# Performance work log

Measured on AMD Instinct MI355X. Metric: run time of the kernel, lower is better.

## Reference

```python
import jax, jax.numpy as jnp
import numpy as np

N = 16384
RANK = 10
IN_F = 64
OUT_F = 64


def setup_inputs() -> dict:
    key = jax.random.key(0)
    k1, k2, k3, k4, k5 = jax.random.split(key, 5)
    return {
        "x": jax.random.normal(k1, (N, IN_F), dtype=jnp.float32),
        "source_embed": jax.random.normal(k2, (N, RANK), dtype=jnp.float32),
        "target_embed": jax.random.normal(k3, (RANK, N), dtype=jnp.float32),
        "W": jax.random.normal(k4, (OUT_F, IN_F), dtype=jnp.float32) * 0.1,
        "b": jax.random.normal(k5, (OUT_F,), dtype=jnp.float32) * 0.1,
    }


def reference(x, source_embed, target_embed, W, b):
    # Learned adjacency: [N, N] = softmax(relu(source @ target), row-wise)
    scores = jax.nn.relu(source_embed @ target_embed)  # [N, N]
    adj = jax.nn.softmax(scores, axis=1)               # [N, N]
    # Graph conv then linear (torch Linear: x @ W.T + b)
    agg = adj @ x                                       # [N, IN_F]
    return agg @ W.T + b                                # [N, OUT_F]
```

## Files before the change

### kernel.cpp

```cpp
#include <hip/hip_runtime.h>


constexpr int N    = 16384;
constexpr int RANK = 10;
constexpr int F    = 64;
constexpr int NH   = N / 2;

typedef float f32x4 __attribute__((ext_vector_type(4)));
typedef short bf16x8 __attribute__((ext_vector_type(8)));

constexpr float LOG2E = 1.4426950408889634f;

static __device__ __forceinline__ float fexp2(float x) {
    float r;
    asm("v_exp_f32 %0, %1" : "=v"(r) : "v"(x));
    return r;
}
static __device__ __forceinline__ unsigned short bfbits(float f) {
    return __builtin_bit_cast(unsigned short, (__bf16)f);
}

__global__ __launch_bounds__(256)
void prep(const float* __restrict__ x, const float* __restrict__ W,
          const float* __restrict__ te,
          uint4* __restrict__ yfrag, uint4* __restrict__ tefrag,
          int js0, int jt0)
{
    const int tid  = threadIdx.x;
    const int lane = tid & 63;
    const int g = lane >> 4, il = lane & 15;

    if (blockIdx.x < 256) {
        __shared__ float xs[32][68];
        const int jl = blockIdx.x;
        const int js = js0 + jl;
#pragma unroll
        for (int i = 0; i < 2; ++i) {
            const int fi = tid * 2 + i;
            const int r = fi >> 4, c4 = fi & 15;
            const float4 v = *reinterpret_cast<const float4*>(x + (size_t)(js * 32 + r) * F + c4 * 4);
            *reinterpret_cast<float4*>(&xs[r][c4 * 4]) = v;
        }
        __syncthreads();
        const int t = tid >> 6;
        const int f = t * 16 + il;
        float y[8];
#pragma unroll
        for (int b = 0; b < 8; ++b) y[b] = 0.f;
        const float* wr = W + f * F;
#pragma unroll
        for (int k4 = 0; k4 < F / 4; ++k4) {
            const float4 wv = *reinterpret_cast<const float4*>(wr + 4 * k4);
#pragma unroll
            for (int b = 0; b < 8; ++b) {
                const int row = 16 * (b >> 2) + 4 * g + (b & 3);
                const float4 xv = *reinterpret_cast<const float4*>(&xs[row][4 * k4]);
                y[b] = fmaf(xv.x, wv.x, y[b]);
                y[b] = fmaf(xv.y, wv.y, y[b]);
                y[b] = fmaf(xv.z, wv.z, y[b]);
                y[b] = fmaf(xv.w, wv.w, y[b]);
            }
        }
        union { unsigned short us[8]; uint4 v; } pk;
#pragma unroll
        for (int b = 0; b < 8; ++b) pk.us[b] = bfbits(y[b]);
        yfrag[(jl * 4 + t) * 64 + lane] = pk.v;
    } else {
        const int lt = (blockIdx.x - 256) * 4 + (tid >> 6);
        const int jt = jt0 + lt;
        union { unsigned short us[8]; uint4 v; } pk;
#pragma unroll
        for (int b = 0; b < 8; ++b) {
            const int k = 8 * g + b;
            unsigned short o = 0;
            if (k < 30) {
                const int band = (k < 10) ? 0 : (k < 20 ? 1 : 2);
                const int r = k - band * 10;
                const float v = te[r * N + jt * 16 + il];
                const __bf16 hb = (__bf16)v;
                o = (band == 2) ? bfbits(v - (float)hb)
                                : __builtin_bit_cast(unsigned short, hb);
            }
            pk.us[b] = o;
        }
        tefrag[lt * 64 + lane] = pk.v;
    }
}

__global__ __launch_bounds__(512, 8)
void gcn_main(const float* __restrict__ se, const uint4* __restrict__ tefrag,
              const uint4* __restrict__ yfrag, const float* __restrict__ bias,
              float* __restrict__ out, float* __restrict__ lsum_self,
              const float* __restrict__ lsum_other, int phase) {
    const int tid  = threadIdx.x;
    const int lane = tid & 63;
    const int wave = tid >> 6;
    const int g = lane >> 4, il = lane & 15;
    const int rowbase = blockIdx.x << 4;

    bf16x8 sef;
    {
        union { unsigned short us[8]; bf16x8 v; } pk;
        const int row = rowbase + il;
#pragma unroll
        for (int b = 0; b < 8; ++b) {
            const int k = 8 * g + b;
            unsigned short o = 0;
            if (k < 30) {
                const int band = (k < 10) ? 0 : (k < 20 ? 1 : 2);
                const int r = k - band * 10;
                const float a = se[row * RANK + r] * LOG2E;
                const __bf16 hb = (__bf16)a;
                o = (band == 1) ? bfbits(a - (float)hb)
                                : __builtin_bit_cast(unsigned short, hb);
            }
            pk.us[b] = o;
        }
        sef = pk.v;
    }

    union { unsigned short us[8]; bf16x8 v; } onesu;
#pragma unroll
    for (int b = 0; b < 8; ++b) onesu.us[b] = 0x3F80;
    const bf16x8 ones = onesu.v;

    f32x4 acc[4];
#pragma unroll
    for (int ft = 0; ft < 4; ++ft) acc[ft] = f32x4{0.f, 0.f, 0.f, 0.f};
    f32x4 accL = {0.f, 0.f, 0.f, 0.f};

    const uint4* tb = tefrag + (size_t)wave * 64 * 64 + lane;
    const uint4* yb = yfrag + (size_t)wave * 32 * 256 + lane;

    for (int s = 0; s < 32; ++s) {
        const uint4 ta0 = tb[0];
        const uint4 ta1 = tb[64];
        const uint4 y0 = yb[0];
        const uint4 y1 = yb[64];
        const uint4 y2 = yb[128];
        const uint4 y3 = yb[192];

        const f32x4 z = {0.f, 0.f, 0.f, 0.f};
        const f32x4 sc0 = __builtin_amdgcn_mfma_f32_16x16x32_bf16(__builtin_bit_cast(bf16x8, ta0), sef, z, 0, 0, 0);
        const f32x4 sc1 = __builtin_amdgcn_mfma_f32_16x16x32_bf16(__builtin_bit_cast(bf16x8, ta1), sef, z, 0, 0, 0);

        union { __bf16 h[8]; bf16x8 v; } af;
#pragma unroll
        for (int q = 0; q < 4; ++q) {
            const float p0 = fexp2(fmaxf(sc0[q], 0.f));
            const float p1 = fexp2(fmaxf(sc1[q], 0.f));
            af.h[q]     = (__bf16)p0;
            af.h[4 + q] = (__bf16)p1;
        }

        acc[0] = __builtin_amdgcn_mfma_f32_16x16x32_bf16(af.v, __builtin_bit_cast(bf16x8, y0), acc[0], 0, 0, 0);
        acc[1] = __builtin_amdgcn_mfma_f32_16x16x32_bf16(af.v, __builtin_bit_cast(bf16x8, y1), acc[1], 0, 0, 0);
        acc[2] = __builtin_amdgcn_mfma_f32_16x16x32_bf16(af.v, __builtin_bit_cast(bf16x8, y2), acc[2], 0, 0, 0);
        acc[3] = __builtin_amdgcn_mfma_f32_16x16x32_bf16(af.v, __builtin_bit_cast(bf16x8, y3), acc[3], 0, 0, 0);
        accL   = __builtin_amdgcn_mfma_f32_16x16x32_bf16(af.v, ones, accL, 0, 0, 0);

        tb += 128;
        yb += 256;
    }

    __shared__ float s_acc[4][1024];
    __shared__ float s_l[8][16];

    if (il == 0) {
#pragma unroll
        for (int q = 0; q < 4; ++q) s_l[wave][4 * g + q] = accL[q];
    }
    if (wave < 4) {
#pragma unroll
        for (int ft = 0; ft < 4; ++ft)
#pragma unroll
            for (int q = 0; q < 4; ++q)
                s_acc[wave][(4 * g + q) * 64 + ft * 16 + il] = acc[ft][q];
    }
    __syncthreads();
    if (wave >= 4) {
#pragma unroll
        for (int ft = 0; ft < 4; ++ft)
#pragma unroll
            for (int q = 0; q < 4; ++q)
                s_acc[wave - 4][(4 * g + q) * 64 + ft * 16 + il] += acc[ft][q];
    }
    __syncthreads();

    if (tid < 256) {
        const int idx  = tid << 2;
        const int row  = idx >> 6;
        const int feat = idx & 63;
        f32x4 v = {0.f, 0.f, 0.f, 0.f};
#pragma unroll
        for (int w = 0; w < 4; ++w) v = v + *reinterpret_cast<const f32x4*>(&s_acc[w][idx]);
        float ls = 0.f;
#pragma unroll
        for (int w = 0; w < 8; ++w) ls += s_l[w][row];

        const int orow = rowbase + row;
        float* op = out + (size_t)orow * F + feat;

        if (phase == 0) {
            if (feat == 0) lsum_self[orow] = ls;
            float4 o; o.x = v[0]; o.y = v[1]; o.z = v[2]; o.w = v[3];
            *reinterpret_cast<float4*>(op) = o;
        } else {
            const float4 prev = *reinterpret_cast<const float4*>(op);
            const float inv = 1.f / (ls + lsum_other[orow]);
            const float4 bv = *reinterpret_cast<const float4*>(bias + feat);
            float4 o;
            o.x = (v[0] + prev.x) * inv + bv.x;
            o.y = (v[1] + prev.y) * inv + bv.y;
            o.z = (v[2] + prev.z) * inv + bv.z;
            o.w = (v[3] + prev.w) * inv + bv.w;
            *reinterpret_cast<float4*>(op) = o;
        }
    }
}

extern "C" void kernel_launch(void* const* d_in, const int* in_sizes, int n_in,
                              void* d_out, int out_size, void* d_ws, size_t ws_size,
                              hipStream_t stream) {
    const float* x  = (const float*)d_in[0];
    const float* se = (const float*)d_in[1];
    const float* te = (const float*)d_in[2];
    const float* W  = (const float*)d_in[3];
    const float* b  = (const float*)d_in[4];
    float* out = (float*)d_out;

    uint4* tefrag = (uint4*)d_ws;
    uint4* yfrag  = (uint4*)((char*)d_ws + (512u << 10));
    float* lsumA  = (float*)((char*)d_ws + (1536u << 10));
    float* lsumB  = lsumA + N;

    prep<<<384, 256, 0, stream>>>(x, W, te, yfrag, tefrag, 0, 0);
    gcn_main<<<N / 16, 512, 0, stream>>>(se, tefrag, yfrag, b, out, lsumA, lsumB, 0);

    prep<<<384, 256, 0, stream>>>(x, W, te, yfrag, tefrag, NH / 32, NH / 16);
    gcn_main<<<N / 16, 512, 0, stream>>>(se, tefrag, yfrag, b, out, lsumB, lsumA, 1);
}
```

Baseline: 188.7 us.

## Process four row tiles per block to reuse loaded target and y fragments

Each block of gcn_main now handles 64 rows (four 16-row tiles) instead of 16, so every loaded tefrag and yfrag fragment feeds four times as many MFMAs. This quarters the grid and the global/L2 traffic for those fragments. In exchange, register use rises (16 accumulators per wave plus four se fragments), occupancy drops (launch bounds relaxed to 2), shared memory grows to about 64KB, and fewer blocks may underfill the GPU.

Result: faster. 151.0 us (-20.0%).

```diff
diff --git a/kernel.cpp b/kernel.cpp
--- a/kernel.cpp
+++ b/kernel.cpp
@@ -87,7 +87,7 @@
     }
 }
 
-__global__ __launch_bounds__(512, 8)
+__global__ __launch_bounds__(512, 2)
 void gcn_main(const float* __restrict__ se, const uint4* __restrict__ tefrag,
               const uint4* __restrict__ yfrag, const float* __restrict__ bias,
               float* __restrict__ out, float* __restrict__ lsum_self,
@@ -96,12 +96,13 @@
     const int lane = tid & 63;
     const int wave = tid >> 6;
     const int g = lane >> 4, il = lane & 15;
-    const int rowbase = blockIdx.x << 4;
-
-    bf16x8 sef;
-    {
+    const int rowbase = blockIdx.x << 6;
+
+    bf16x8 sef[4];
+#pragma unroll
+    for (int rt = 0; rt < 4; ++rt) {
         union { unsigned short us[8]; bf16x8 v; } pk;
-        const int row = rowbase + il;
+        const int row = rowbase + rt * 16 + il;
 #pragma unroll
         for (int b = 0; b < 8; ++b) {
             const int k = 8 * g + b;
@@ -116,7 +117,7 @@
             }
             pk.us[b] = o;
         }
-        sef = pk.v;
+        sef[rt] = pk.v;
     }
 
     union { unsigned short us[8]; bf16x8 v; } onesu;
@@ -124,10 +125,14 @@
     for (int b = 0; b < 8; ++b) onesu.us[b] = 0x3F80;
     const bf16x8 ones = onesu.v;
 
-    f32x4 acc[4];
-#pragma unroll
-    for (int ft = 0; ft < 4; ++ft) acc[ft] = f32x4{0.f, 0.f, 0.f, 0.f};
-    f32x4 accL = {0.f, 0.f, 0.f, 0.f};
+    f32x4 acc[4][4];
+#pragma unroll
+    for (int rt = 0; rt < 4; ++rt)
+#pragma unroll
+        for (int ft = 0; ft < 4; ++ft) acc[rt][ft] = f32x4{0.f, 0.f, 0.f, 0.f};
+    f32x4 accL[4];
+#pragma unroll
+    for (int rt = 0; rt < 4; ++rt) accL[rt] = f32x4{0.f, 0.f, 0.f, 0.f};
 
     const uint4* tb = tefrag + (size_t)wave * 64 * 64 + lane;
     const uint4* yb = yfrag + (size_t)wave * 32 * 256 + lane;
@@ -139,83 +144,101 @@
         const uint4 y1 = yb[64];
         const uint4 y2 = yb[128];
         const uint4 y3 = yb[192];
-
         const f32x4 z = {0.f, 0.f, 0.f, 0.f};
-        const f32x4 sc0 = __builtin_amdgcn_mfma_f32_16x16x32_bf16(__builtin_bit_cast(bf16x8, ta0), sef, z, 0, 0, 0);
-        const f32x4 sc1 = __builtin_amdgcn_mfma_f32_16x16x32_bf16(__builtin_bit_cast(bf16x8, ta1), sef, z, 0, 0, 0);
-
-        union { __bf16 h[8]; bf16x8 v; } af;
-#pragma unroll
-        for (int q = 0; q < 4; ++q) {
-            const float p0 = fexp2(fmaxf(sc0[q], 0.f));
-            const float p1 = fexp2(fmaxf(sc1[q], 0.f));
-            af.h[q]     = (__bf16)p0;
-            af.h[4 + q] = (__bf16)p1;
-        }
-
-        acc[0] = __builtin_amdgcn_mfma_f32_16x16x32_bf16(af.v, __builtin_bit_cast(bf16x8, y0), acc[0], 0, 0, 0);
-        acc[1] = __builtin_amdgcn_mfma_f32_16x16x32_bf16(af.v, __builtin_bit_cast(bf16x8, y1), acc[1], 0, 0, 0);
-        acc[2] = __builtin_amdgcn_mfma_f32_16x16x32_bf16(af.v, __builtin_bit_cast(bf16x8, y2), acc[2], 0, 0, 0);
-        acc[3] = __builtin_amdgcn_mfma_f32_16x16x32_bf16(af.v, __builtin_bit_cast(bf16x8, y3), acc[3], 0, 0, 0);
-        accL   = __builtin_amdgcn_mfma_f32_16x16x32_bf16(af.v, ones, accL, 0, 0, 0);
+
+#pragma unroll
+        for (int rt = 0; rt < 4; ++rt) {
+            const f32x4 sc0 = __builtin_amdgcn_mfma_f32_16x16x32_bf16(__builtin_bit_cast(bf16x8, ta0), sef[rt], z, 0, 0, 0);
+            const f32x4 sc1 = __builtin_amdgcn_mfma_f32_16x16x32_bf16(__builtin_bit_cast(bf16x8, ta1), sef[rt], z, 0, 0, 0);
+
+            union { __bf16 h[8]; bf16x8 v; } af;
+#pragma unroll
+            for (int q = 0; q < 4; ++q) {
+                af.h[q]     = (__bf16)fexp2(fmaxf(sc0[q], 0.f));
+                af.h[4 + q] = (__bf16)fexp2(fmaxf(sc1[q], 0.f));
+            }
+
+            acc[rt][0] = __builtin_amdgcn_mfma_f32_16x16x32_bf16(af.v, __builtin_bit_cast(bf16x8, y0), acc[rt][0], 0, 0, 0);
+            acc[rt][1] = __builtin_amdgcn_mfma_f32_16x16x32_bf16(af.v, __builtin_bit_cast(bf16x8, y1), acc[rt][1], 0, 0, 0);
+            acc[rt][2] = __builtin_amdgcn_mfma_f32_16x16x32_bf16(af.v, __builtin_bit_cast(bf16x8, y2), acc[rt][2], 0, 0, 0);
+            acc[rt][3] = __builtin_amdgcn_mfma_f32_16x16x32_bf16(af.v, __builtin_bit_cast(bf16x8, y3), acc[rt][3], 0, 0, 0);
+            accL[rt]   = __builtin_amdgcn_mfma_f32_16x16x32_bf16(af.v, ones, accL[rt], 0, 0, 0);
+        }
 
         tb += 128;
         yb += 256;
     }
 
-    __shared__ float s_acc[4][1024];
-    __shared__ float s_l[8][16];
+    __shared__ float s_acc[4][4096];
+    __shared__ float s_l[8][64];
 
     if (il == 0) {
 #pragma unroll
-        for (int q = 0; q < 4; ++q) s_l[wave][4 * g + q] = accL[q];
+        for (int rt = 0; rt < 4; ++rt)
+#pragma unroll
+            for (int q = 0; q < 4; ++q) s_l[wave][rt * 16 + 4 * g + q] = accL[rt][q];
     }
     if (wave < 4) {
 #pragma unroll
-        for (int ft = 0; ft < 4; ++ft)
-#pragma unroll
-            for (int q = 0; q < 4; ++q)
-                s_acc[wave][(4 * g + q) * 64 + ft * 16 + il] = acc[ft][q];
+        for (int rt = 0; rt < 4; ++rt)
+#pragma unroll
+            for (int ft = 0; ft < 4; ++ft)
+#pragma unroll
+                for (int q = 0; q < 4; ++q)
+                    s_acc[wave][(rt * 16 + 4 * g + q) * 64 + ft * 16 + il] = acc[rt][ft][q];
     }
     __syncthreads();
     if (wave >= 4) {
 #pragma unroll
-        for (int ft = 0; ft < 4; ++ft)
-#pragma unroll
-            for (int q = 0; q < 4; ++q)
-                s_acc[wave - 4][(4 * g + q) * 64 + ft * 16 + il] += acc[ft][q];
+        for (int rt = 0; rt < 4; ++rt)
+#pragma unroll
+            for (int ft = 0; ft < 4; ++ft)
+#pragma unroll
+                for (int q = 0; q < 4; ++q)
+                    s_acc[wave - 4][(rt * 16 + 4 * g + q) * 64 + ft * 16 + il] += acc[rt][ft][q];
     }
     __syncthreads();
 
-    if (tid < 256) {
-        const int idx  = tid << 2;
-        const int row  = idx >> 6;
-        const int feat = idx & 63;
-        f32x4 v = {0.f, 0.f, 0.f, 0.f};
-#pragma unroll
-        for (int w = 0; w < 4; ++w) v = v + *reinterpret_cast<const f32x4*>(&s_acc[w][idx]);
-        float ls = 0.f;
-#pragma unroll
-        for (int w = 0; w < 8; ++w) ls += s_l[w][row];
-
-        const int orow = rowbase + row;
-        float* op = out + (size_t)orow * F + feat;
-
-        if (phase == 0) {
-            if (feat == 0) lsum_self[orow] = ls;
-            float4 o; o.x = v[0]; o.y = v[1]; o.z = v[2]; o.w = v[3];
-            *reinterpret_cast<float4*>(op) = o;
-        } else {
-            const float4 prev = *reinterpret_cast<const float4*>(op);
-            const float inv = 1.f / (ls + lsum_other[orow]);
-            const float4 bv = *reinterpret_cast<const float4*>(bias + feat);
-            float4 o;
-            o.x = (v[0] + prev.x) * inv + bv.x;
-            o.y = (v[1] + prev.y) * inv + bv.y;
-            o.z = (v[2] + prev.z) * inv + bv.z;
-            o.w = (v[3] + prev.w) * inv + bv.w;
-            *reinterpret_cast<float4*>(op) = o;
-        }
+    const int e    = tid << 3;
+    const int row  = e >> 6;
+    const int feat = e & 63;
+    f32x4 v0 = {0.f, 0.f, 0.f, 0.f}, v1 = {0.f, 0.f, 0.f, 0.f};
+#pragma unroll
+    for (int w = 0; w < 4; ++w) {
+        v0 = v0 + *reinterpret_cast<const f32x4*>(&s_acc[w][row * 64 + feat]);
+        v1 = v1 + *reinterpret_cast<const f32x4*>(&s_acc[w][row * 64 + feat + 4]);
+    }
+    float ls = 0.f;
+#pragma unroll
+    for (int w = 0; w < 8; ++w) ls += s_l[w][row];
+
+    const int orow = rowbase + row;
+    float* op = out + (size_t)orow * F + feat;
+
+    if (phase == 0) {
+        if (feat == 0) lsum_self[orow] = ls;
+        float4 o0, o1;
+        o0.x = v0[0]; o0.y = v0[1]; o0.z = v0[2]; o0.w = v0[3];
+        o1.x = v1[0]; o1.y = v1[1]; o1.z = v1[2]; o1.w = v1[3];
+        *reinterpret_cast<float4*>(op)     = o0;
+        *reinterpret_cast<float4*>(op + 4) = o1;
+    } else {
+        const float4 p0 = *reinterpret_cast<const float4*>(op);
+        const float4 p1 = *reinterpret_cast<const float4*>(op + 4);
+        const float inv = 1.f / (ls + lsum_other[orow]);
+        const float4 b0 = *reinterpret_cast<const float4*>(bias + feat);
+        const float4 b1 = *reinterpret_cast<const float4*>(bias + feat + 4);
+        float4 o0, o1;
+        o0.x = (v0[0] + p0.x) * inv + b0.x;
+        o0.y = (v0[1] + p0.y) * inv + b0.y;
+        o0.z = (v0[2] + p0.z) * inv + b0.z;
+        o0.w = (v0[3] + p0.w) * inv + b0.w;
+        o1.x = (v1[0] + p1.x) * inv + b1.x;
+        o1.y = (v1[1] + p1.y) * inv + b1.y;
+        o1.z = (v1[2] + p1.z) * inv + b1.z;
+        o1.w = (v1[3] + p1.w) * inv + b1.w;
+        *reinterpret_cast<float4*>(op)     = o0;
+        *reinterpret_cast<float4*>(op + 4) = o1;
     }
 }
 
@@ -235,8 +258,8 @@
     float* lsumB  = lsumA + N;
 
     prep<<<384, 256, 0, stream>>>(x, W, te, yfrag, tefrag, 0, 0);
-    gcn_main<<<N / 16, 512, 0, stream>>>(se, tefrag, yfrag, b, out, lsumA, lsumB, 0);
+    gcn_main<<<N / 64, 512, 0, stream>>>(se, tefrag, yfrag, b, out, lsumA, lsumB, 0);
 
     prep<<<384, 256, 0, stream>>>(x, W, te, yfrag, tefrag, NH / 32, NH / 16);
-    gcn_main<<<N / 16, 512, 0, stream>>>(se, tefrag, yfrag, b, out, lsumB, lsumA, 1);
-}
+    gcn_main<<<N / 64, 512, 0, stream>>>(se, tefrag, yfrag, b, out, lsumB, lsumA, 1);
+}
```
